# Kernel optimization log

Measured on AMD Instinct MI355X. Metric: run time of the kernel, lower is better.

## Reference

```python
import jax, jax.numpy as jnp
import numpy as np

N_JOINTS = 24


def rotation_6d_to_matrix(d6):
    """Zhou et al. 6D -> 3x3 rotation. d6: [..., 6] -> [..., 3, 3] (rows b1,b2,b3)."""
    a1, a2 = d6[..., :3], d6[..., 3:]
    b1 = a1 / jnp.linalg.norm(a1, axis=-1, keepdims=True)
    b2 = a2 - jnp.sum(b1 * a2, axis=-1, keepdims=True) * b1
    b2 = b2 / jnp.linalg.norm(b2, axis=-1, keepdims=True)
    b3 = jnp.cross(b1, b2)
    return jnp.stack([b1, b2, b3], axis=-2)


def setup_inputs() -> dict:
    key = jax.random.key(0)
    k1, k2 = jax.random.split(key)
    N = 131072
    angles = jax.random.normal(k1, (N, N_JOINTS, 6), dtype=jnp.float32)
    xyz = jax.random.normal(k2, (1, N_JOINTS, 3), dtype=jnp.float32)
    # simple chain kinematic tree in topological order
    parent_idx = jnp.arange(0, N_JOINTS - 1, dtype=jnp.int64)
    child_idx = jnp.arange(1, N_JOINTS, dtype=jnp.int64)
    return {"angles": angles, "xyz": xyz, "parent_idx": parent_idx, "child_idx": child_idx}


def reference(angles, xyz, parent_idx, child_idx):
    rot = rotation_6d_to_matrix(angles)  # [N, J, 3, 3]
    N = rot.shape[0]
    dtype = rot.dtype
    parent = np.asarray(parent_idx)
    child = np.asarray(child_idx)
    xyz0 = xyz[0]  # [J, 3] reference skeleton
    bottom = jnp.broadcast_to(jnp.array([0.0, 0.0, 0.0, 1.0], dtype=dtype), (N, 1, 4))

    def make_m(r, t):
        # r: [N,3,3], t: [3] -> homogeneous [N,4,4] with translation r @ t
        trans = jnp.einsum('nij,j->ni', r, t)  # [N,3]
        top = jnp.concatenate([r, trans[..., None]], axis=-1)  # [N,3,4]
        return jnp.concatenate([top, bottom], axis=-2)

    M = [None] * N_JOINTS
    M[0] = make_m(rot[:, 0], xyz0[0])
    for p, c in zip(parent, child):
        p, c = int(p), int(c)
        M[c] = M[p] @ make_m(rot[:, c], xyz0[c] - xyz0[p])
    return jnp.stack(M, axis=1)[..., :3, 3]  # [N, J, 3]
```

## Files before the change

kernel.cpp:

```cpp
#include <hip/hip_runtime.h>
#include <stdint.h>


#define N_JOINTS 24
#define SAMPLES_PER_BLOCK 32
#define BLOCK_THREADS 128

typedef float v4f __attribute__((ext_vector_type(4)));
typedef float v2f __attribute__((ext_vector_type(2)));

__global__ __launch_bounds__(BLOCK_THREADS, 4) void fk_kernel(
    const v4f* __restrict__ ain,
    const float* __restrict__ xyz,
    v4f* __restrict__ aout)
{
    __shared__ v4f  s_buf[SAMPLES_PER_BLOCK * 37];
    __shared__ float s_t[N_JOINTS * 3];

    const int tid = threadIdx.x;

    if (tid < N_JOINTS) {
        float x = xyz[tid * 3 + 0];
        float y = xyz[tid * 3 + 1];
        float z = xyz[tid * 3 + 2];
        if (tid > 0) {
            x -= xyz[(tid - 1) * 3 + 0];
            y -= xyz[(tid - 1) * 3 + 1];
            z -= xyz[(tid - 1) * 3 + 2];
        }
        s_t[tid * 3 + 0] = x; s_t[tid * 3 + 1] = y; s_t[tid * 3 + 2] = z;
    }

    const size_t in_base = (size_t)blockIdx.x * (SAMPLES_PER_BLOCK * 36);
    #pragma unroll
    for (int it = 0; it < 9; ++it) {
        const int g = tid + BLOCK_THREADS * it;
        const int s = g / 36;
        const int r = g - s * 36;
        s_buf[s * 37 + r] = __builtin_nontemporal_load(&ain[in_base + g]);
    }
    __syncthreads();

    const int s   = tid >> 2;
    const int seg = tid & 3;
    const v4f* __restrict__ row = &s_buf[s * 37 + seg * 9];

    float R[9], t[3];
    float o[18];

    #pragma unroll
    for (int p = 0; p < 3; ++p) {
        const v4f v0 = row[p * 3 + 0];
        const v4f v1 = row[p * 3 + 1];
        const v4f v2 = row[p * 3 + 2];
        float d6[12];
        d6[0] = v0.x; d6[1] = v0.y; d6[2]  = v0.z; d6[3]  = v0.w;
        d6[4] = v1.x; d6[5] = v1.y; d6[6]  = v1.z; d6[7]  = v1.w;
        d6[8] = v2.x; d6[9] = v2.y; d6[10] = v2.z; d6[11] = v2.w;

        #pragma unroll
        for (int h = 0; h < 2; ++h) {
            const int jl = p * 2 + h;
            const int j  = seg * 6 + jl;
            const float a1x = d6[h * 6 + 0], a1y = d6[h * 6 + 1], a1z = d6[h * 6 + 2];
            const float a2x = d6[h * 6 + 3], a2y = d6[h * 6 + 4], a2z = d6[h * 6 + 5];

            const float inv1 = rsqrtf(a1x * a1x + a1y * a1y + a1z * a1z);
            const float b1x = a1x * inv1, b1y = a1y * inv1, b1z = a1z * inv1;
            const float dd = b1x * a2x + b1y * a2y + b1z * a2z;
            float b2x = a2x - dd * b1x, b2y = a2y - dd * b1y, b2z = a2z - dd * b1z;
            const float inv2 = rsqrtf(b2x * b2x + b2y * b2y + b2z * b2z);
            b2x *= inv2; b2y *= inv2; b2z *= inv2;
            const float b3x = b1y * b2z - b1z * b2y;
            const float b3y = b1z * b2x - b1x * b2z;
            const float b3z = b1x * b2y - b1y * b2x;
            const float Rj[9] = { b1x, b1y, b1z,  b2x, b2y, b2z,  b3x, b3y, b3z };

            const float tx = s_t[j * 3 + 0], ty = s_t[j * 3 + 1], tz = s_t[j * 3 + 2];
            const float tlx = Rj[0] * tx + Rj[1] * ty + Rj[2] * tz;
            const float tly = Rj[3] * tx + Rj[4] * ty + Rj[5] * tz;
            const float tlz = Rj[6] * tx + Rj[7] * ty + Rj[8] * tz;

            if (jl == 0) {
                #pragma unroll
                for (int k = 0; k < 9; ++k) R[k] = Rj[k];
                t[0] = tlx; t[1] = tly; t[2] = tlz;
            } else {
                t[0] += R[0] * tlx + R[1] * tly + R[2] * tlz;
                t[1] += R[3] * tlx + R[4] * tly + R[5] * tlz;
                t[2] += R[6] * tlx + R[7] * tly + R[8] * tlz;
                float Nn[9];
                #pragma unroll
                for (int r2 = 0; r2 < 3; ++r2)
                    #pragma unroll
                    for (int c = 0; c < 3; ++c)
                        Nn[r2 * 3 + c] = R[r2 * 3 + 0] * Rj[0 * 3 + c]
                                       + R[r2 * 3 + 1] * Rj[1 * 3 + c]
                                       + R[r2 * 3 + 2] * Rj[2 * 3 + c];
                #pragma unroll
                for (int k = 0; k < 9; ++k) R[k] = Nn[k];
            }
            o[jl * 3 + 0] = t[0];
            o[jl * 3 + 1] = t[1];
            o[jl * 3 + 2] = t[2];
        }
    }

    #pragma unroll
    for (int d = 1; d <= 2; d *= 2) {
        float LR[9], Lt[3];
        #pragma unroll
        for (int k = 0; k < 9; ++k) LR[k] = __shfl_up(R[k], (unsigned)d);
        #pragma unroll
        for (int c = 0; c < 3; ++c) Lt[c] = __shfl_up(t[c], (unsigned)d);
        if (seg >= d) {
            float nt0 = Lt[0] + LR[0] * t[0] + LR[1] * t[1] + LR[2] * t[2];
            float nt1 = Lt[1] + LR[3] * t[0] + LR[4] * t[1] + LR[5] * t[2];
            float nt2 = Lt[2] + LR[6] * t[0] + LR[7] * t[1] + LR[8] * t[2];
            float Nn[9];
            #pragma unroll
            for (int r2 = 0; r2 < 3; ++r2)
                #pragma unroll
                for (int c = 0; c < 3; ++c)
                    Nn[r2 * 3 + c] = LR[r2 * 3 + 0] * R[0 * 3 + c]
                                   + LR[r2 * 3 + 1] * R[1 * 3 + c]
                                   + LR[r2 * 3 + 2] * R[2 * 3 + c];
            #pragma unroll
            for (int k = 0; k < 9; ++k) R[k] = Nn[k];
            t[0] = nt0; t[1] = nt1; t[2] = nt2;
        }
    }

    float ER[9], Et[3];
    #pragma unroll
    for (int k = 0; k < 9; ++k) ER[k] = __shfl_up(R[k], 1u);
    #pragma unroll
    for (int c = 0; c < 3; ++c) Et[c] = __shfl_up(t[c], 1u);
    if (seg == 0) {
        ER[0] = 1.f; ER[1] = 0.f; ER[2] = 0.f;
        ER[3] = 0.f; ER[4] = 1.f; ER[5] = 0.f;
        ER[6] = 0.f; ER[7] = 0.f; ER[8] = 1.f;
        Et[0] = 0.f; Et[1] = 0.f; Et[2] = 0.f;
    }

    #pragma unroll
    for (int k = 0; k < 6; ++k) {
        const float ox = o[3 * k + 0], oy = o[3 * k + 1], oz = o[3 * k + 2];
        o[3 * k + 0] = Et[0] + ER[0] * ox + ER[1] * oy + ER[2] * oz;
        o[3 * k + 1] = Et[1] + ER[3] * ox + ER[4] * oy + ER[5] * oz;
        o[3 * k + 2] = Et[2] + ER[6] * ox + ER[7] * oy + ER[8] * oz;
    }

    __syncthreads();
    v2f* ob = reinterpret_cast<v2f*>(s_buf);
    #pragma unroll
    for (int q = 0; q < 9; ++q) {
        v2f v; v.x = o[2 * q + 0]; v.y = o[2 * q + 1];
        ob[tid * 9 + q] = v;
    }
    __syncthreads();

    const size_t out_base = (size_t)blockIdx.x * (SAMPLES_PER_BLOCK * 18);
    #pragma unroll
    for (int it = 0; it < 4; ++it)
        __builtin_nontemporal_store(s_buf[tid + BLOCK_THREADS * it],
                                    &aout[out_base + tid + BLOCK_THREADS * it]);
    if (tid < 64)
        __builtin_nontemporal_store(s_buf[512 + tid],
                                    &aout[out_base + 512 + tid]);
}

extern "C" void kernel_launch(void* const* d_in, const int* in_sizes, int n_in,
                              void* d_out, int out_size, void* d_ws, size_t ws_size,
                              hipStream_t stream) {
    const float* angles = (const float*)d_in[0];
    const float* xyz    = (const float*)d_in[1];
    float* out = (float*)d_out;

    const int N = in_sizes[0] / (N_JOINTS * 6);
    const int grid = N / SAMPLES_PER_BLOCK;
    fk_kernel<<<grid, BLOCK_THREADS, 0, stream>>>(
        reinterpret_cast<const v4f*>(angles), xyz,
        reinterpret_cast<v4f*>(out));
}
```

Baseline: 25.13 us.

## Process two sample tiles per block with second tile prefetched into registers

```diff
diff --git a/kernel.cpp b/kernel.cpp
--- a/kernel.cpp
+++ b/kernel.cpp
@@ -3,50 +3,18 @@
 
 
 #define N_JOINTS 24
-#define SAMPLES_PER_BLOCK 32
-#define BLOCK_THREADS 128
+#define SPB 32
+#define BT  128
 
 typedef float v4f __attribute__((ext_vector_type(4)));
 typedef float v2f __attribute__((ext_vector_type(2)));
 
-__global__ __launch_bounds__(BLOCK_THREADS, 4) void fk_kernel(
-    const v4f* __restrict__ ain,
-    const float* __restrict__ xyz,
-    v4f* __restrict__ aout)
+__device__ __forceinline__ void compute_tile(
+    const v4f* __restrict__ row,
+    const float* __restrict__ st,
+    int seg, float* __restrict__ o)
 {
-    __shared__ v4f  s_buf[SAMPLES_PER_BLOCK * 37];
-    __shared__ float s_t[N_JOINTS * 3];
-
-    const int tid = threadIdx.x;
-
-    if (tid < N_JOINTS) {
-        float x = xyz[tid * 3 + 0];
-        float y = xyz[tid * 3 + 1];
-        float z = xyz[tid * 3 + 2];
-        if (tid > 0) {
-            x -= xyz[(tid - 1) * 3 + 0];
-            y -= xyz[(tid - 1) * 3 + 1];
-            z -= xyz[(tid - 1) * 3 + 2];
-        }
-        s_t[tid * 3 + 0] = x; s_t[tid * 3 + 1] = y; s_t[tid * 3 + 2] = z;
-    }
-
-    const size_t in_base = (size_t)blockIdx.x * (SAMPLES_PER_BLOCK * 36);
-    #pragma unroll
-    for (int it = 0; it < 9; ++it) {
-        const int g = tid + BLOCK_THREADS * it;
-        const int s = g / 36;
-        const int r = g - s * 36;
-        s_buf[s * 37 + r] = __builtin_nontemporal_load(&ain[in_base + g]);
-    }
-    __syncthreads();
-
-    const int s   = tid >> 2;
-    const int seg = tid & 3;
-    const v4f* __restrict__ row = &s_buf[s * 37 + seg * 9];
-
     float R[9], t[3];
-    float o[18];
 
     #pragma unroll
     for (int p = 0; p < 3; ++p) {
@@ -76,7 +44,7 @@
             const float b3z = b1x * b2y - b1y * b2x;
             const float Rj[9] = { b1x, b1y, b1z,  b2x, b2y, b2z,  b3x, b3y, b3z };
 
-            const float tx = s_t[j * 3 + 0], ty = s_t[j * 3 + 1], tz = s_t[j * 3 + 2];
+            const float tx = st[j * 3 + 0], ty = st[j * 3 + 1], tz = st[j * 3 + 2];
             const float tlx = Rj[0] * tx + Rj[1] * ty + Rj[2] * tz;
             const float tly = Rj[3] * tx + Rj[4] * ty + Rj[5] * tz;
             const float tlz = Rj[6] * tx + Rj[7] * ty + Rj[8] * tz;
@@ -150,24 +118,105 @@
         o[3 * k + 1] = Et[1] + ER[3] * ox + ER[4] * oy + ER[5] * oz;
         o[3 * k + 2] = Et[2] + ER[6] * ox + ER[7] * oy + ER[8] * oz;
     }
-
-    __syncthreads();
-    v2f* ob = reinterpret_cast<v2f*>(s_buf);
-    #pragma unroll
-    for (int q = 0; q < 9; ++q) {
-        v2f v; v.x = o[2 * q + 0]; v.y = o[2 * q + 1];
-        ob[tid * 9 + q] = v;
-    }
-    __syncthreads();
-
-    const size_t out_base = (size_t)blockIdx.x * (SAMPLES_PER_BLOCK * 18);
-    #pragma unroll
-    for (int it = 0; it < 4; ++it)
-        __builtin_nontemporal_store(s_buf[tid + BLOCK_THREADS * it],
-                                    &aout[out_base + tid + BLOCK_THREADS * it]);
-    if (tid < 64)
-        __builtin_nontemporal_store(s_buf[512 + tid],
-                                    &aout[out_base + 512 + tid]);
+}
+
+__global__ __launch_bounds__(BT, 4) void fk_kernel(
+    const v4f* __restrict__ ain,
+    const float* __restrict__ xyz,
+    v4f* __restrict__ aout)
+{
+    __shared__ v4f   s_buf[SPB * 37];
+    __shared__ float s_t[N_JOINTS * 3];
+
+    const int tid = threadIdx.x;
+
+    if (tid < N_JOINTS) {
+        float x = xyz[tid * 3 + 0];
+        float y = xyz[tid * 3 + 1];
+        float z = xyz[tid * 3 + 2];
+        if (tid > 0) {
+            x -= xyz[(tid - 1) * 3 + 0];
+            y -= xyz[(tid - 1) * 3 + 1];
+            z -= xyz[(tid - 1) * 3 + 2];
+        }
+        s_t[tid * 3 + 0] = x; s_t[tid * 3 + 1] = y; s_t[tid * 3 + 2] = z;
+    }
+
+    const int s   = tid >> 2;
+    const int seg = tid & 3;
+
+    const size_t base = (size_t)blockIdx.x * 2304;
+
+    v4f va[9], vb[9];
+    #pragma unroll
+    for (int k = 0; k < 9; ++k)
+        va[k] = __builtin_nontemporal_load(&ain[base + tid + BT * k]);
+    #pragma unroll
+    for (int k = 0; k < 9; ++k)
+        vb[k] = __builtin_nontemporal_load(&ain[base + 1152 + tid + BT * k]);
+
+    #pragma unroll
+    for (int k = 0; k < 9; ++k) {
+        const int g  = tid + BT * k;
+        const int s2 = g / 36;
+        const int r  = g - s2 * 36;
+        s_buf[s2 * 37 + r] = va[k];
+    }
+    __syncthreads();
+
+    float oA[18];
+    compute_tile(&s_buf[s * 37 + seg * 9], s_t, seg, oA);
+    __syncthreads();
+
+    {
+        v2f* ob = reinterpret_cast<v2f*>(s_buf);
+        #pragma unroll
+        for (int q = 0; q < 9; ++q) {
+            v2f vv; vv.x = oA[2 * q + 0]; vv.y = oA[2 * q + 1];
+            ob[tid * 9 + q] = vv;
+        }
+        __syncthreads();
+        const size_t ob4 = (size_t)blockIdx.x * 1152;
+        #pragma unroll
+        for (int it = 0; it < 4; ++it)
+            __builtin_nontemporal_store(s_buf[tid + BT * it],
+                                        &aout[ob4 + tid + BT * it]);
+        if (tid < 64)
+            __builtin_nontemporal_store(s_buf[512 + tid],
+                                        &aout[ob4 + 512 + tid]);
+    }
+    __syncthreads();
+
+    #pragma unroll
+    for (int k = 0; k < 9; ++k) {
+        const int g  = tid + BT * k;
+        const int s2 = g / 36;
+        const int r  = g - s2 * 36;
+        s_buf[s2 * 37 + r] = vb[k];
+    }
+    __syncthreads();
+
+    float oB[18];
+    compute_tile(&s_buf[s * 37 + seg * 9], s_t, seg, oB);
+    __syncthreads();
+
+    {
+        v2f* ob = reinterpret_cast<v2f*>(s_buf);
+        #pragma unroll
+        for (int q = 0; q < 9; ++q) {
+            v2f vv; vv.x = oB[2 * q + 0]; vv.y = oB[2 * q + 1];
+            ob[tid * 9 + q] = vv;
+        }
+        __syncthreads();
+        const size_t ob4 = (size_t)blockIdx.x * 1152 + 576;
+        #pragma unroll
+        for (int it = 0; it < 4; ++it)
+            __builtin_nontemporal_store(s_buf[tid + BT * it],
+                                        &aout[ob4 + tid + BT * it]);
+        if (tid < 64)
+            __builtin_nontemporal_store(s_buf[512 + tid],
+                                        &aout[ob4 + 512 + tid]);
+    }
 }
 
 extern "C" void kernel_launch(void* const* d_in, const int* in_sizes, int n_in,
@@ -178,8 +227,8 @@
     float* out = (float*)d_out;
 
     const int N = in_sizes[0] / (N_JOINTS * 6);
-    const int grid = N / SAMPLES_PER_BLOCK;
-    fk_kernel<<<grid, BLOCK_THREADS, 0, stream>>>(
+    const int grid = N / (SPB * 2);
+    fk_kernel<<<grid, BT, 0, stream>>>(
         reinterpret_cast<const v4f*>(angles), xyz,
         reinterpret_cast<v4f*>(out));
 }
```

Result: slower. 30.39 us (+20.9%).
